# Optimization experiments

Hardware: AMD Instinct MI355X
Metric: run time of the kernel (lower is better)

Reference implementation:

```python
import jax, jax.numpy as jnp
import numpy as np

NUM_HEADS = 16
KV_CHANNELS = 128
MASK_FILL = -10000.0  # TE attention_mask_func fill value


def setup_inputs() -> dict:
    key = jax.random.key(0)
    k1, k2, k3 = jax.random.split(key, 3)
    S, B, H = 2048, 2, 2048
    hidden_states = jax.random.normal(k1, (S, B, H), dtype=jnp.float32)
    attention_mask = jnp.zeros((B, 1, S, S), dtype=bool)  # True = masked out
    qkv_weight = jax.random.normal(k2, (H, 3 * H), dtype=jnp.float32) * (1.0 / np.sqrt(H))
    qkv_bias = jnp.zeros((3 * H,), dtype=jnp.float32)
    proj_weight = jax.random.normal(k3, (H, H), dtype=jnp.float32) * (1.0 / np.sqrt(H))
    proj_bias = jnp.zeros((H,), dtype=jnp.float32)
    return {
        "hidden_states": hidden_states,
        "attention_mask": attention_mask,
        "qkv_weight": qkv_weight,
        "qkv_bias": qkv_bias,
        "proj_weight": proj_weight,
        "proj_bias": proj_bias,
    }


def reference(hidden_states, attention_mask, qkv_weight, qkv_bias, proj_weight, proj_bias):
    S, B, H = hidden_states.shape
    nh, d = NUM_HEADS, KV_CHANNELS
    # QKV GEMM: [s,b,H] @ [H,3H] -> [s,b,3H] -> [s,b,nh,3d] -> split
    mixed = hidden_states @ qkv_weight + qkv_bias
    mixed = mixed.reshape(S, B, nh, 3 * d)
    q, k, v = jnp.split(mixed, 3, axis=-1)  # each [s,b,nh,d]
    # BMM1 with 1/sqrt(d) scaling (layer_number=None -> no layer scaling)
    norm_factor = jnp.asarray(np.sqrt(d), dtype=hidden_states.dtype)
    scores = jnp.einsum("sbhd,tbhd->bhst", q, k) / norm_factor  # [b,nh,s,s]
    # causal mask (future positions masked) OR'd with provided bool padding mask
    causal = ~jnp.tril(jnp.ones((S, S), dtype=bool))  # True above diagonal
    mask = jnp.logical_or(causal[None, None], attention_mask)
    scores = jnp.where(mask, jnp.asarray(MASK_FILL, scores.dtype), scores)
    probs = jax.nn.softmax(scores, axis=-1)
    # dropout is identity in eval mode (training=False)
    # BMM2: [b,nh,s,t] x [t,b,nh,d] -> [s,b,nh,d] -> [s,b,H]
    context = jnp.einsum("bhst,tbhd->sbhd", probs, v).reshape(S, B, H)
    # output projection; TE Dense(use_bias=False, return_bias=True) returns bias
    out = context @ proj_weight
    return out, proj_bias
```

## Files before the change

### kernel.cpp

```cpp
#include <hip/hip_runtime.h>
#include <cstdint>
#include <math.h>

#define S_LEN 2048
#define BATCH 2
#define HID   2048
#define NHEAD 16
#define DHEAD 128

typedef _Float16 h8 __attribute__((ext_vector_type(8)));
typedef _Float16 h4 __attribute__((ext_vector_type(4)));
typedef float f32x4 __attribute__((ext_vector_type(4)));

__device__ __forceinline__ void gload16(const void* g, void* l) {
  __builtin_amdgcn_global_load_lds(
      (const __attribute__((address_space(1))) unsigned int*)g,
      (__attribute__((address_space(3))) unsigned int*)l, 16, 0, 0);
}

template <bool HAS_BIAS, bool OUT_HALF>
__global__ __launch_bounds__(512) void gemm_256v2(
    const _Float16* __restrict__ A, const _Float16* __restrict__ Bt,
    const float* __restrict__ bias, void* __restrict__ Cout, int M, int N,
    int K) {
  __shared__ _Float16 LA[2][16384];
  __shared__ _Float16 LB[2][16384];
  const int tid = (int)threadIdx.x;
  const int wave = tid >> 6, lane = tid & 63;
  const int ln = lane & 15, quad = lane >> 4;
  const int wm = wave >> 2, wn = wave & 3;
  const int bm = (int)blockIdx.y * 256, bn = (int)blockIdx.x * 256;
  const int NT = K >> 6;

  const int gc8 = ((lane & 7) ^ (lane >> 3)) * 8;
  const int rbase = wave * 8 + (lane >> 3);
  uint32_t oA[4], oB[4];
#pragma unroll
  for (int q = 0; q < 4; q++) {
    oA[q] = (uint32_t)(bm + q * 64 + rbase) * (uint32_t)K + (uint32_t)gc8;
    oB[q] = (uint32_t)(bn + q * 64 + rbase) * (uint32_t)K + (uint32_t)gc8;
  }

#define STAGEA(bb_, u_)                                                  \
  {                                                                      \
    _Pragma("unroll") for (int q = 0; q < 4; q++)                        \
        gload16(A + (oA[q] + (uint32_t)(u_)*64u),                        \
                &LA[bb_][q * 4096 + wave * 512]);                        \
  }
#define STAGEB(bb_, u_)                                                  \
  {                                                                      \
    _Pragma("unroll") for (int q = 0; q < 4; q++)                        \
        gload16(Bt + (oB[q] + (uint32_t)(u_)*64u),                       \
                &LB[bb_][q * 4096 + wave * 512]);                        \
  }

  const int arow = ln * 64;
  const int sc0 = ((quad ^ (ln & 7))) * 8;
  const int sc1 = (((4 + quad) ^ (ln & 7))) * 8;
  const int abase = wm * 8192;
  const int bbase = wn * 4096;

  f32x4 acc[8][4];
#pragma unroll
  for (int m = 0; m < 8; m++)
#pragma unroll
    for (int n = 0; n < 4; n++) acc[m][n] = (f32x4){0.f, 0.f, 0.f, 0.f};
  h8 aF[4][2], bF[4][2];

#define HALF(mo_)                                                            \
  _Pragma("unroll") for (int mm_ = 0; mm_ < 4; mm_++)                        \
      _Pragma("unroll") for (int nn_ = 0; nn_ < 4; nn_++) {                  \
    acc[(mo_) + mm_][nn_] = __builtin_amdgcn_mfma_f32_16x16x32_f16(          \
        aF[mm_][0], bF[nn_][0], acc[(mo_) + mm_][nn_], 0, 0, 0);             \
    acc[(mo_) + mm_][nn_] = __builtin_amdgcn_mfma_f32_16x16x32_f16(          \
        aF[mm_][1], bF[nn_][1], acc[(mo_) + mm_][nn_], 0, 0, 0);             \
  }

  STAGEA(0, 0) STAGEB(0, 0)
  STAGEA(1, 1) STAGEB(1, 1)
  asm volatile("s_waitcnt vmcnt(8)" ::: "memory");
  __builtin_amdgcn_s_barrier();

  for (int u = 0; u < NT; ++u) {
    const int bb = u & 1;

#pragma unroll
    for (int m = 0; m < 4; m++) {
      aF[m][0] = *(const h8*)&LA[bb][abase + m * 1024 + arow + sc0];
      aF[m][1] = *(const h8*)&LA[bb][abase + m * 1024 + arow + sc1];
    }
#pragma unroll
    for (int n = 0; n < 4; n++) {
      bF[n][0] = *(const h8*)&LB[bb][bbase + n * 1024 + arow + sc0];
      bF[n][1] = *(const h8*)&LB[bb][bbase + n * 1024 + arow + sc1];
    }
    __builtin_amdgcn_s_barrier();
    __builtin_amdgcn_s_setprio(1);
    HALF(0)
    __builtin_amdgcn_s_setprio(0);
    __builtin_amdgcn_s_barrier();

#pragma unroll
    for (int m = 0; m < 4; m++) {
      aF[m][0] = *(const h8*)&LA[bb][abase + (m + 4) * 1024 + arow + sc0];
      aF[m][1] = *(const h8*)&LA[bb][abase + (m + 4) * 1024 + arow + sc1];
    }
    if (u + 2 < NT) {
      STAGEA(bb, u + 2) STAGEB(bb, u + 2)
      asm volatile("s_waitcnt vmcnt(8)" ::: "memory");
    } else if (u + 1 < NT) {
      asm volatile("s_waitcnt vmcnt(0)" ::: "memory");
    }
    __builtin_amdgcn_s_barrier();
    __builtin_amdgcn_s_setprio(1);
    HALF(4)
    __builtin_amdgcn_s_setprio(0);
    __builtin_amdgcn_s_barrier();
  }
#undef HALF
#undef STAGEA
#undef STAGEB

#pragma unroll
  for (int m = 0; m < 8; m++) {
#pragma unroll
    for (int r = 0; r < 4; r++) {
      const size_t row = (size_t)(bm + wm * 128 + m * 16 + quad * 4 + r);
#pragma unroll
      for (int n = 0; n < 4; n++) {
        const int col = bn + wn * 64 + n * 16 + ln;
        float v = acc[m][n][r];
        if (HAS_BIAS) v += bias[col];
        if (OUT_HALF)
          ((_Float16*)Cout)[row * N + col] = (_Float16)v;
        else
          ((float*)Cout)[row * N + col] = v;
      }
    }
  }
}

template <bool HAS_BIAS, bool OUT_HALF>
__global__ __launch_bounds__(512) void gemm_128(
    const _Float16* __restrict__ A, const _Float16* __restrict__ Bt,
    const float* __restrict__ bias, void* __restrict__ Cout, int M, int N,
    int K) {
  __shared__ _Float16 LA[2][8192];
  __shared__ _Float16 LB[2][16384];
  const int tid = (int)threadIdx.x;
  const int wave = tid >> 6, lane = tid & 63;
  const int ln = lane & 15, quad = lane >> 4;
  const int wm = wave >> 2, wn = wave & 3;
  const int bm = (int)blockIdx.y * 128, bn = (int)blockIdx.x * 256;
  const int NT = K >> 6;

  const int gc8 = ((lane & 7) ^ (lane >> 3)) * 8;
  const uint32_t oA0 =
      (uint32_t)(bm + wave * 8 + (lane >> 3)) * (uint32_t)K + (uint32_t)gc8;
  const uint32_t oA1 = oA0 + (uint32_t)(64 * K);
  const uint32_t oB00 =
      (uint32_t)(bn + wave * 16 + (lane >> 3)) * (uint32_t)K + (uint32_t)gc8;
  const uint32_t oB01 = oB00 + (uint32_t)(8 * K);
  const uint32_t oB10 = oB00 + (uint32_t)(128 * K);
  const uint32_t oB11 = oB10 + (uint32_t)(8 * K);

#define STAGE128(bb_, u_)                                                    \
  {                                                                          \
    gload16(A + (oA0 + (uint32_t)(u_)*64u), &LA[bb_][wave * 512]);           \
    gload16(A + (oA1 + (uint32_t)(u_)*64u), &LA[bb_][4096 + wave * 512]);    \
    gload16(Bt + (oB00 + (uint32_t)(u_)*64u), &LB[bb_][wave * 1024]);        \
    gload16(Bt + (oB01 + (uint32_t)(u_)*64u), &LB[bb_][wave * 1024 + 512]);  \
    gload16(Bt + (oB10 + (uint32_t)(u_)*64u), &LB[bb_][8192 + wave * 1024]); \
    gload16(Bt + (oB11 + (uint32_t)(u_)*64u),                                \
            &LB[bb_][8192 + wave * 1024 + 512]);                             \
  }

  const int arow = ln * 64;
  const int sc0 = ((quad ^ (ln & 7))) * 8;
  const int sc1 = (((4 + quad) ^ (ln & 7))) * 8;
  const int abase = wm * 4096;
  const int bbase = wn * 4096;

  f32x4 acc[4][4];
#pragma unroll
  for (int m = 0; m < 4; m++)
#pragma unroll
    for (int n = 0; n < 4; n++) acc[m][n] = (f32x4){0.f, 0.f, 0.f, 0.f};
  h8 aF[4][2], bF[4][2];

#define HQUAD(n0_)                                                           \
  _Pragma("unroll") for (int mm_ = 0; mm_ < 4; mm_++)                        \
      _Pragma("unroll") for (int nn_ = 0; nn_ < 2; nn_++) {                  \
    acc[mm_][(n0_) + nn_] = __builtin_amdgcn_mfma_f32_16x16x32_f16(          \
        aF[mm_][0], bF[(n0_) + nn_][0], acc[mm_][(n0_) + nn_], 0, 0, 0);     \
    acc[mm_][(n0_) + nn_] = __builtin_amdgcn_mfma_f32_16x16x32_f16(          \
        aF[mm_][1], bF[(n0_) + nn_][1], acc[mm_][(n0_) + nn_], 0, 0, 0);     \
  }

  STAGE128(0, 0)
  STAGE128(1, 1)
  asm volatile("s_waitcnt vmcnt(6)" ::: "memory");
  __builtin_amdgcn_s_barrier();

  for (int u = 0; u < NT; ++u) {
    const int bb = u & 1;

#pragma unroll
    for (int m = 0; m < 4; m++) {
      aF[m][0] = *(const h8*)&LA[bb][abase + m * 1024 + arow + sc0];
      aF[m][1] = *(const h8*)&LA[bb][abase + m * 1024 + arow + sc1];
    }
#pragma unroll
    for (int n = 0; n < 2; n++) {
      bF[n][0] = *(const h8*)&LB[bb][bbase + n * 1024 + arow + sc0];
      bF[n][1] = *(const h8*)&LB[bb][bbase + n * 1024 + arow + sc1];
    }
    __builtin_amdgcn_s_barrier();
    __builtin_amdgcn_s_setprio(1);
    HQUAD(0)
    __builtin_amdgcn_s_setprio(0);
    __builtin_amdgcn_s_barrier();

#pragma unroll
    for (int n = 2; n < 4; n++) {
      bF[n][0] = *(const h8*)&LB[bb][bbase + n * 1024 + arow + sc0];
      bF[n][1] = *(const h8*)&LB[bb][bbase + n * 1024 + arow + sc1];
    }
    if (u + 2 < NT) {
      STAGE128(bb, u + 2)
      asm volatile("s_waitcnt vmcnt(6)" ::: "memory");
    } else if (u + 1 < NT) {
      asm volatile("s_waitcnt vmcnt(0)" ::: "memory");
    }
    __builtin_amdgcn_s_barrier();
    __builtin_amdgcn_s_setprio(1);
    HQUAD(2)
    __builtin_amdgcn_s_setprio(0);
    __builtin_amdgcn_s_barrier();
  }
#undef HQUAD
#undef STAGE128

#pragma unroll
  for (int m = 0; m < 4; m++) {
#pragma unroll
    for (int r = 0; r < 4; r++) {
      const size_t row = (size_t)(bm + wm * 64 + m * 16 + quad * 4 + r);
#pragma unroll
      for (int n = 0; n < 4; n++) {
        const int col = bn + wn * 64 + n * 16 + ln;
        float v = acc[m][n][r];
        if (HAS_BIAS) v += bias[col];
        if (OUT_HALF)
          ((_Float16*)Cout)[row * N + col] = (_Float16)v;
        else
          ((float*)Cout)[row * N + col] = v;
      }
    }
  }
}

__global__ __launch_bounds__(256) void transpose_cvt(
    const float* __restrict__ in, _Float16* __restrict__ out, int K, int N) {
  __shared__ float t[64][65];
  const int bn = blockIdx.x * 64, bk = blockIdx.y * 64;
  const int tid = (int)threadIdx.x;
  {
    const int r0 = tid >> 4, c4 = (tid & 15) * 4;
#pragma unroll
    for (int i = 0; i < 4; i++) {
      const int r = r0 + 16 * i;
      float4 v = *(const float4*)&in[(size_t)(bk + r) * N + bn + c4];
      t[r][c4] = v.x;
      t[r][c4 + 1] = v.y;
      t[r][c4 + 2] = v.z;
      t[r][c4 + 3] = v.w;
    }
  }
  __syncthreads();
  {
    const int c0 = tid >> 4, r4 = (tid & 15) * 4;
#pragma unroll
    for (int i = 0; i < 4; i++) {
      const int c = c0 + 16 * i;
      h4 o = {(_Float16)t[r4][c], (_Float16)t[r4 + 1][c],
              (_Float16)t[r4 + 2][c], (_Float16)t[r4 + 3][c]};
      *(h4*)&out[(size_t)(bn + c) * K + bk + r4] = o;
    }
  }
}

__global__ __launch_bounds__(256) void cvt_fp16(const float* __restrict__ in,
                                                _Float16* __restrict__ out,
                                                int n4) {
  int i = blockIdx.x * blockDim.x + threadIdx.x;
  if (i < n4) {
    float4 v = ((const float4*)in)[i];
    h4 o = {(_Float16)v.x, (_Float16)v.y, (_Float16)v.z, (_Float16)v.w};
    *(h4*)&out[4 * (size_t)i] = o;
  }
}

__global__ __launch_bounds__(256) void pack_mask(
    const unsigned char* __restrict__ m, uint32_t* __restrict__ pm) {
  const int i = blockIdx.x * 256 + threadIdx.x;
  const int w = i & 63, r = (i >> 6) & (S_LEN - 1), b = i >> 17;
  const uint32_t* src =
      (const uint32_t*)(m + ((size_t)b * S_LEN + r) * S_LEN + w * 32);
  uint32_t bits = 0;
#pragma unroll
  for (int k = 0; k < 8; k++) {
    const uint32_t v = src[k];
    bits |= ((v & 0x000000FFu) ? 1u : 0u) << (4 * k);
    bits |= ((v & 0x0000FF00u) ? 1u : 0u) << (4 * k + 1);
    bits |= ((v & 0x00FF0000u) ? 1u : 0u) << (4 * k + 2);
    bits |= ((v & 0xFF000000u) ? 1u : 0u) << (4 * k + 3);
  }
  const int c0 = w * 32;
  uint32_t caus;
  if (c0 > r) {
    caus = 0xFFFFFFFFu;
  } else if (r - c0 >= 31) {
    caus = 0u;
  } else {
    caus = ~((2u << (r - c0)) - 1u);
  }
  pm[i] = bits | caus;
}

__global__ __launch_bounds__(256) void pack_kv(
    const _Float16* __restrict__ mixed, _Float16* __restrict__ KP,
    _Float16* __restrict__ VP) {
  __shared__ _Float16 Tv[128 * 40];
  const int kt = blockIdx.x;
  const int z = blockIdx.y;
  const int kb = kt * 32;
  const int tid = threadIdx.x;
  const size_t RS = (size_t)BATCH * NHEAD * 384;
  const _Float16* base = mixed + (size_t)z * 384;

  {
    const int r = tid >> 3, d0 = (tid & 7) * 16;
    const _Float16* src = base + (size_t)(kb + r) * RS + 256 + d0;
    h8 v0 = *(const h8*)src;
    h8 v1 = *(const h8*)(src + 8);
#pragma unroll
    for (int e = 0; e < 8; e++) Tv[(d0 + e) * 40 + r] = v0[e];
#pragma unroll
    for (int e = 0; e < 8; e++) Tv[(d0 + 8 + e) * 40 + r] = v1[e];
  }
  __syncthreads();

  const size_t tb = ((size_t)z * 64 + kt) * 8 * 512;
#pragma unroll
  for (int c = 0; c < 2; c++) {
    const int idx = tid + 256 * c;
    const int i = idx >> 6, l = idx & 63;
    const int ln = l & 15, quad = l >> 4;
    {
      const int jn = i >> 2, kq = i & 3;
      h8 v = *(const h8*)(base + (size_t)(kb + 16 * jn + ln) * RS + 128 +
                          32 * kq + 8 * quad);
      *(h8*)&KP[tb + (size_t)i * 512 + l * 8] = v;
    }
    {
      h8 v = *(const h8*)&Tv[(16 * i + ln) * 40 + 8 * quad];
      *(h8*)&VP[tb + (size_t)i * 512 + l * 8] = v;
    }
  }
}

__global__ __launch_bounds__(256) void flash_attn_v8(
    const _Float16* __restrict__ mixed, const _Float16* __restrict__ KP,
    const _Float16* __restrict__ VP, const uint32_t* __restrict__ pmask,
    _Float16* __restrict__ ctx) {
  const int qt = (int)gridDim.x - 1 - (int)blockIdx.x;
  const int h = blockIdx.y, b = blockIdx.z;
  const int z = b * NHEAD + h;
  const int qb = qt * 64;
  const int tid = threadIdx.x;
  const int wave = tid >> 6, lane = tid & 63;
  const int ln = lane & 15, quad = lane >> 4;

  __shared__ _Float16 Kbuf[2][8 * 512];
  __shared__ _Float16 Vbuf[2][8 * 512];
  __shared__ _Float16 St[4][16 * 40];

  const size_t RS = (size_t)BATCH * NHEAD * 384;
  const _Float16* base = mixed + (size_t)z * 384;
  const uint32_t* pmb = pmask + (size_t)b * S_LEN * 64;
  const float scale = 0.08838834764831845f;

  h8 qfrag[4];
  {
    const size_t row = (size_t)(qb + 16 * wave + ln);
#pragma unroll
    for (int kq = 0; kq < 4; kq++) {
      h8 v = *(const h8*)(base + row * RS + 32 * kq + 8 * quad);
#pragma unroll
      for (int j = 0; j < 8; j++) v[j] = (_Float16)((float)v[j] * scale);
      qfrag[kq] = v;
    }
  }

  f32x4 o[8];
#pragma unroll
  for (int nt = 0; nt < 8; nt++) o[nt] = (f32x4){0.f, 0.f, 0.f, 0.f};
  float lpart[4] = {0.f, 0.f, 0.f, 0.f};

  const int ntiles = 2 * qt + 2;

  const size_t zt = (size_t)z * 64;
#define STAGE(kt_, buf_)                                                   \
  {                                                                        \
    const size_t tbk = (zt + (kt_)) * (8 * 512) + lane * 8;                \
    _Pragma("unroll") for (int c = 0; c < 2; c++) {                        \
      const int ch = 2 * wave + c;                                         \
      gload16(KP + tbk + ch * 512, &Kbuf[buf_][ch * 512]);                 \
      gload16(VP + tbk + ch * 512, &Vbuf[buf_][ch * 512]);                 \
    }                                                                      \
  }

  STAGE(0, 0)

  const uint32_t* pmr = pmb + (size_t)(qb + 16 * wave + 4 * quad) * 64;

  for (int kt = 0; kt < ntiles; kt++) {
    const int cur = kt & 1;
    __syncthreads();

    if (kt + 1 < ntiles) STAGE(kt + 1, cur ^ 1)

    uint32_t mw[4];
#pragma unroll
    for (int r = 0; r < 4; r++) mw[r] = pmr[(size_t)r * 64 + kt];

    f32x4 s[2];
    s[0] = (f32x4){0.f, 0.f, 0.f, 0.f};
    s[1] = (f32x4){0.f, 0.f, 0.f, 0.f};
#pragma unroll
    for (int kq = 0; kq < 4; kq++) {
#pragma unroll
      for (int jn = 0; jn < 2; jn++) {
        h8 bk = *(const h8*)&Kbuf[cur][(jn * 4 + kq) * 512 + lane * 8];
        s[jn] = __builtin_amdgcn_mfma_f32_16x16x32_f16(qfrag[kq], bk, s[jn], 0,
                                                       0, 0);
      }
    }

#pragma unroll
    for (int r = 0; r < 4; r++) {
      const uint32_t ms = mw[r] >> ln;
#pragma unroll
      for (int jn = 0; jn < 2; jn++) {
        const float sv = ((ms >> (16 * jn)) & 1u) ? -10000.0f : s[jn][r];
        const float p = __expf(sv);
        lpart[r] += p;
        St[wave][(4 * quad + r) * 40 + 16 * jn + ln] = (_Float16)p;
      }
    }
    __threadfence_block();

    {
      h8 ap = *(const h8*)&St[wave][ln * 40 + 8 * quad];
#pragma unroll
      for (int nt = 0; nt < 8; nt++) {
        h8 bv = *(const h8*)&Vbuf[cur][nt * 512 + lane * 8];
        o[nt] = __builtin_amdgcn_mfma_f32_16x16x32_f16(ap, bv, o[nt], 0, 0, 0);
      }
    }
  }
#undef STAGE

#pragma unroll
  for (int r = 0; r < 4; r++) {
    float l = lpart[r];
#pragma unroll
    for (int off = 8; off >= 1; off >>= 1) l += __shfl_xor(l, off, 16);
    const float inv_l = 1.0f / l;
    const size_t row_g = (size_t)(qb + 16 * wave + 4 * quad + r);
    _Float16* dst = ctx + (row_g * BATCH + b) * HID + h * DHEAD;
#pragma unroll
    for (int nt = 0; nt < 8; nt++)
      dst[16 * nt + ln] = (_Float16)(o[nt][r] * inv_l);
  }
}

__global__ void copy_bias(const float* __restrict__ src,
                          float* __restrict__ dst) {
  int i = blockIdx.x * blockDim.x + threadIdx.x;
  if (i < HID) dst[i] = src[i];
}

extern "C" void kernel_launch(void* const* d_in, const int* in_sizes, int n_in,
                              void* d_out, int out_size, void* d_ws,
                              size_t ws_size, hipStream_t stream) {
  (void)in_sizes;
  (void)n_in;
  const float* hs = (const float*)d_in[0];
  const unsigned char* mask = (const unsigned char*)d_in[1];
  const float* qkv_w = (const float*)d_in[2];
  const float* qkv_b = (const float*)d_in[3];
  const float* proj_w = (const float*)d_in[4];
  const float* proj_b = (const float*)d_in[5];
  float* out = (float*)d_out;

  const size_t M = (size_t)S_LEN * BATCH;
  const size_t mixed_e = M * 3 * HID;
  const size_t qkvwt_e = (size_t)3 * HID * HID;
  const size_t hsh_e = M * HID;
  const size_t projwt_e = (size_t)HID * HID;
  const size_t ctx_e = M * HID;
  const size_t need =
      (mixed_e + qkvwt_e + hsh_e + projwt_e + ctx_e) * sizeof(_Float16);
  if (ws_size < need) return;

  _Float16* mixed = (_Float16*)d_ws;
  _Float16* qkv_wt = mixed + mixed_e;
  _Float16* hs_h = qkv_wt + qkvwt_e;
  _Float16* proj_wt = hs_h + hsh_e;
  _Float16* ctx = proj_wt + projwt_e;
  _Float16* KP = hs_h;
  _Float16* VP = qkv_wt;
  uint32_t* pmask = (uint32_t*)out;

  cvt_fp16<<<(int)(hsh_e / 4 / 256), 256, 0, stream>>>(hs, hs_h,
                                                       (int)(hsh_e / 4));
  transpose_cvt<<<dim3(3 * HID / 64, HID / 64), 256, 0, stream>>>(
      qkv_w, qkv_wt, HID, 3 * HID);
  transpose_cvt<<<dim3(HID / 64, HID / 64), 256, 0, stream>>>(
      proj_w, proj_wt, HID, HID);
  pack_mask<<<(BATCH * S_LEN * 64) / 256, 256, 0, stream>>>(mask, pmask);

  gemm_256v2<true, true><<<dim3(3 * HID / 256, M / 256), 512, 0, stream>>>(
      hs_h, qkv_wt, qkv_b, mixed, (int)M, 3 * HID, HID);

  pack_kv<<<dim3(S_LEN / 32, BATCH * NHEAD), 256, 0, stream>>>(mixed, KP, VP);

  flash_attn_v8<<<dim3(S_LEN / 64, NHEAD, BATCH), 256, 0, stream>>>(
      mixed, KP, VP, pmask, ctx);

  gemm_128<false, false><<<dim3(HID / 256, M / 128), 512, 0, stream>>>(
      ctx, proj_wt, nullptr, out, (int)M, HID, HID);

  copy_bias<<<(HID + 255) / 256, 256, 0, stream>>>(proj_b, out + M * HID);
}
```

Before: 451.4 us.

## Enlarge attention blocks to 128 queries with remapped grid; split QKV GEMM tiles

The flash attention kernel now uses 512-thread blocks covering 128 query rows, so K/V tiles staged in shared memory are reused by twice as many waves. A 1D grid is remapped so that blocks sharing a head sit close together and the longest causal blocks are scheduled first. The QKV GEMM is split into a 256-tile launch over the first 4096 columns plus a 128-tile launch over the rest, aiming at better wave quantization across CUs. Larger attention blocks may lower occupancy and raise causal load imbalance.

Result: faster. 414.2 us (-8.2%).

```diff
diff --git a/kernel.cpp b/kernel.cpp
--- a/kernel.cpp
+++ b/kernel.cpp
@@ -370,21 +370,23 @@
   }
 }
 
-__global__ __launch_bounds__(256) void flash_attn_v8(
+__global__ __launch_bounds__(512) void flash_attn_v9(
     const _Float16* __restrict__ mixed, const _Float16* __restrict__ KP,
     const _Float16* __restrict__ VP, const uint32_t* __restrict__ pmask,
     _Float16* __restrict__ ctx) {
-  const int qt = (int)gridDim.x - 1 - (int)blockIdx.x;
-  const int h = blockIdx.y, b = blockIdx.z;
-  const int z = b * NHEAD + h;
-  const int qb = qt * 64;
+  const int bid = (int)blockIdx.x;
+  const int x = bid & 7, s = bid >> 3;
+  const int z = x * 4 + (s & 3);
+  const int qt = 15 - (s >> 2);
+  const int h = z & (NHEAD - 1), b = z >> 4;
+  const int qb = qt * 128;
   const int tid = threadIdx.x;
   const int wave = tid >> 6, lane = tid & 63;
   const int ln = lane & 15, quad = lane >> 4;
 
   __shared__ _Float16 Kbuf[2][8 * 512];
   __shared__ _Float16 Vbuf[2][8 * 512];
-  __shared__ _Float16 St[4][16 * 40];
+  __shared__ _Float16 St[8][16 * 40];
 
   const size_t RS = (size_t)BATCH * NHEAD * 384;
   const _Float16* base = mixed + (size_t)z * 384;
@@ -408,17 +410,14 @@
   for (int nt = 0; nt < 8; nt++) o[nt] = (f32x4){0.f, 0.f, 0.f, 0.f};
   float lpart[4] = {0.f, 0.f, 0.f, 0.f};
 
-  const int ntiles = 2 * qt + 2;
+  const int ntiles = 4 * qt + 4;
 
   const size_t zt = (size_t)z * 64;
-#define STAGE(kt_, buf_)                                                   \
-  {                                                                        \
-    const size_t tbk = (zt + (kt_)) * (8 * 512) + lane * 8;                \
-    _Pragma("unroll") for (int c = 0; c < 2; c++) {                        \
-      const int ch = 2 * wave + c;                                         \
-      gload16(KP + tbk + ch * 512, &Kbuf[buf_][ch * 512]);                 \
-      gload16(VP + tbk + ch * 512, &Vbuf[buf_][ch * 512]);                 \
-    }                                                                      \
+#define STAGE(kt_, buf_)                                            \
+  {                                                                 \
+    const size_t tbk = (zt + (kt_)) * (8 * 512) + lane * 8;         \
+    gload16(KP + tbk + wave * 512, &Kbuf[buf_][wave * 512]);        \
+    gload16(VP + tbk + wave * 512, &Vbuf[buf_][wave * 512]);        \
   }
 
   STAGE(0, 0)
@@ -435,16 +434,16 @@
 #pragma unroll
     for (int r = 0; r < 4; r++) mw[r] = pmr[(size_t)r * 64 + kt];
 
-    f32x4 s[2];
-    s[0] = (f32x4){0.f, 0.f, 0.f, 0.f};
-    s[1] = (f32x4){0.f, 0.f, 0.f, 0.f};
+    f32x4 sreg[2];
+    sreg[0] = (f32x4){0.f, 0.f, 0.f, 0.f};
+    sreg[1] = (f32x4){0.f, 0.f, 0.f, 0.f};
 #pragma unroll
     for (int kq = 0; kq < 4; kq++) {
 #pragma unroll
       for (int jn = 0; jn < 2; jn++) {
         h8 bk = *(const h8*)&Kbuf[cur][(jn * 4 + kq) * 512 + lane * 8];
-        s[jn] = __builtin_amdgcn_mfma_f32_16x16x32_f16(qfrag[kq], bk, s[jn], 0,
-                                                       0, 0);
+        sreg[jn] = __builtin_amdgcn_mfma_f32_16x16x32_f16(qfrag[kq], bk,
+                                                          sreg[jn], 0, 0, 0);
       }
     }
 
@@ -453,7 +452,8 @@
       const uint32_t ms = mw[r] >> ln;
 #pragma unroll
       for (int jn = 0; jn < 2; jn++) {
-        const float sv = ((ms >> (16 * jn)) & 1u) ? -10000.0f : s[jn][r];
+        const float sv =
+            ((ms >> (16 * jn)) & 1u) ? -10000.0f : sreg[jn][r];
         const float p = __expf(sv);
         lpart[r] += p;
         St[wave][(4 * quad + r) * 40 + 16 * jn + ln] = (_Float16)p;
@@ -532,13 +532,15 @@
       proj_w, proj_wt, HID, HID);
   pack_mask<<<(BATCH * S_LEN * 64) / 256, 256, 0, stream>>>(mask, pmask);
 
-  gemm_256v2<true, true><<<dim3(3 * HID / 256, M / 256), 512, 0, stream>>>(
+  gemm_256v2<true, true><<<dim3(16, (int)(M / 256)), 512, 0, stream>>>(
       hs_h, qkv_wt, qkv_b, mixed, (int)M, 3 * HID, HID);
+  gemm_128<true, true><<<dim3(8, (int)(M / 128)), 512, 0, stream>>>(
+      hs_h, qkv_wt + (size_t)4096 * HID, qkv_b + 4096,
+      (void*)(mixed + 4096), (int)M, 3 * HID, HID);
 
   pack_kv<<<dim3(S_LEN / 32, BATCH * NHEAD), 256, 0, stream>>>(mixed, KP, VP);
 
-  flash_attn_v8<<<dim3(S_LEN / 64, NHEAD, BATCH), 256, 0, stream>>>(
-      mixed, KP, VP, pmask, ctx);
+  flash_attn_v9<<<512, 512, 0, stream>>>(mixed, KP, VP, pmask, ctx);
 
   gemm_128<false, false><<<dim3(HID / 256, M / 128), 512, 0, stream>>>(
       ctx, proj_wt, nullptr, out, (int)M, HID, HID);
```
